# Kernel tuning notes

Measured on AMD Instinct MI355X. Metric: run time of the kernel, lower is better.

Reference implementation:

```python
import jax, jax.numpy as jnp
import numpy as np

D_MODEL = 1024
N_HEADS = 16
D_K = D_MODEL // N_HEADS


def setup_inputs() -> dict:
    key = jax.random.key(0)
    ks = jax.random.split(key, 7)
    B, S, D = 2, 2048, D_MODEL
    scale = 1.0 / np.sqrt(D)
    return {
        "query": jax.random.normal(ks[0], (B, S, D), dtype=jnp.float32),
        "key": jax.random.normal(ks[1], (B, S, D), dtype=jnp.float32),
        "value": jax.random.normal(ks[2], (B, S, D), dtype=jnp.float32),
        "w_q": jax.random.normal(ks[3], (D, D), dtype=jnp.float32) * scale,
        "w_k": jax.random.normal(ks[4], (D, D), dtype=jnp.float32) * scale,
        "w_v": jax.random.normal(ks[5], (D, D), dtype=jnp.float32) * scale,
        "w_o": jax.random.normal(ks[6], (D, D), dtype=jnp.float32) * scale,
    }


def reference(query, key, value, w_q, w_k, w_v, w_o):
    B, S, D = query.shape
    H, Dk = N_HEADS, D_K
    # nn.Linear (no bias): x @ W.T ; then split heads -> [B, H, S, Dk]
    def split_heads(x, W):
        return (x @ W.T).reshape(B, S, H, Dk).transpose(0, 2, 1, 3)
    Q = split_heads(query, w_q)
    K = split_heads(key, w_k)
    V = split_heads(value, w_v)
    scores = jnp.einsum("bhqd,bhkd->bhqk", Q, K) / np.sqrt(Dk).astype(jnp.float32)
    attn = jax.nn.softmax(scores, axis=-1)  # dropout is identity in eval
    attended = jnp.einsum("bhqk,bhkd->bhqd", attn, V)
    attended = attended.transpose(0, 2, 1, 3).reshape(B, S, D)
    output = attended @ w_o.T
    avg_attention = attn.mean(axis=1)  # mean over heads -> [B, S, S]
    return (output, avg_attention)
```

## Files before the change

### kernel.cpp

```cpp
#include <hip/hip_runtime.h>
#include <math.h>

#define SEQ 2048
#define DMODEL 1024
#define NH 16
#define DK 64
#define BATCH 2

using bf16x8 = __attribute__((ext_vector_type(8))) __bf16;
using bf16x4 = __attribute__((ext_vector_type(4))) __bf16;
using f32x4  = __attribute__((ext_vector_type(4))) float;

__device__ inline f32x4 mfma16(bf16x8 a, bf16x8 b, f32x4 c) {
    return __builtin_amdgcn_mfma_f32_16x16x32_bf16(a, b, c, 0, 0, 0);
}

__device__ inline void load_lds16(const void* g, void* l) {
    __builtin_amdgcn_global_load_lds(
        (const __attribute__((address_space(1))) void*)g,
        (__attribute__((address_space(3))) void*)l, 16, 0, 0);
}

#define EXP_SCALE 0.18033688011112042f

__global__ __launch_bounds__(256) void conv_bf16(
        const float* __restrict__ q, const float* __restrict__ k,
        const float* __restrict__ v, const float* __restrict__ wq,
        const float* __restrict__ wk, const float* __restrict__ wv,
        const float* __restrict__ wo,
        __bf16* __restrict__ oq, __bf16* __restrict__ ok, __bf16* __restrict__ ov,
        __bf16* __restrict__ owq, __bf16* __restrict__ owk,
        __bf16* __restrict__ owv, __bf16* __restrict__ owo) {
    int bid = blockIdx.x;
    const float* src;
    __bf16* dst;
    size_t off;
    if (bid < 3072) {
        int ti = bid >> 10;
        src = ti == 0 ? q : (ti == 1 ? k : v);
        dst = ti == 0 ? oq : (ti == 1 ? ok : ov);
        off = (size_t)(bid & 1023) * 4096;
    } else {
        int ti = (bid - 3072) >> 8;
        src = ti == 0 ? wq : (ti == 1 ? wk : (ti == 2 ? wv : wo));
        dst = ti == 0 ? owq : (ti == 1 ? owk : (ti == 2 ? owv : owo));
        off = (size_t)((bid - 3072) & 255) * 4096;
    }
    src += off; dst += off;
    const int t = threadIdx.x;
#pragma unroll
    for (int i = 0; i < 4; ++i) {
        float4 x = *(const float4*)(src + t * 4 + i * 1024);
        bf16x4 y;
        y[0] = (__bf16)x.x; y[1] = (__bf16)x.y;
        y[2] = (__bf16)x.z; y[3] = (__bf16)x.w;
        *(bf16x4*)(dst + t * 4 + i * 1024) = y;
    }
}

__device__ __forceinline__ void gemm_core(const __bf16* __restrict__ A,
                                          const __bf16* __restrict__ B,
                                          void* __restrict__ out, int mode,
                                          int m0, int n0, int N,
                                          __bf16* As, __bf16* Bs) {
    const int t    = threadIdx.x;
    const int w    = t >> 6;
    const int lane = t & 63;
    const int m    = lane & 15;
    const int kg   = lane >> 4;
    const int wr   = w >> 1, wc = w & 1;

    f32x4 acc[4][2] = {};

    for (int k0 = 0; k0 < 1024; k0 += 64) {
        __syncthreads();
#pragma unroll
        for (int i = 0; i < 4; ++i) {
            const int ablk = w * 4 + i;
            const int mt = ablk >> 1, kt = ablk & 1;
            const __bf16* ga = A + (size_t)(m0 + mt * 16 + m) * 1024 + k0 + kt * 32 + kg * 8;
            load_lds16(ga, &As[ablk * 512]);
        }
#pragma unroll
        for (int i = 0; i < 2; ++i) {
            const int bblk = w * 2 + i;
            const int nt = bblk >> 1, kt = bblk & 1;
            const __bf16* gb = B + (size_t)(n0 + nt * 16 + m) * 1024 + k0 + kt * 32 + kg * 8;
            load_lds16(gb, &Bs[bblk * 512]);
        }
        __syncthreads();
#pragma unroll
        for (int kt = 0; kt < 2; ++kt) {
            bf16x8 af[4], bg[2];
#pragma unroll
            for (int i = 0; i < 4; ++i)
                af[i] = *(const bf16x8*)&As[((wr * 4 + i) * 2 + kt) * 512 + lane * 8];
#pragma unroll
            for (int j = 0; j < 2; ++j)
                bg[j] = *(const bf16x8*)&Bs[((wc * 2 + j) * 2 + kt) * 512 + lane * 8];
#pragma unroll
            for (int i = 0; i < 4; ++i)
#pragma unroll
                for (int j = 0; j < 2; ++j)
                    acc[i][j] = mfma16(af[i], bg[j], acc[i][j]);
        }
    }

#pragma unroll
    for (int i = 0; i < 4; ++i) {
        const int rb = m0 + wr * 64 + i * 16 + kg * 4;
#pragma unroll
        for (int j = 0; j < 2; ++j) {
            const int gc = n0 + wc * 32 + j * 16 + m;
#pragma unroll
            for (int r = 0; r < 4; ++r) {
                const int gr = rb + r;
                const float vv = acc[i][j][r];
                if (mode == 0) {
                    ((float*)out)[(size_t)gr * N + gc] = vv;
                } else if (mode == 1) {
                    ((__bf16*)out)[(size_t)gr * N + gc] = (__bf16)vv;
                } else {
                    const int hh = gr >> 6, dd = gr & 63;
                    const int bb = gc >> 11, ss = gc & 2047;
                    ((__bf16*)out)[(((size_t)bb * NH + hh) * DK + dd) * SEQ + ss] = (__bf16)vv;
                }
            }
        }
    }
}

__device__ __forceinline__ int xcd_swz(int s, int cpx) {
    return (s & 7) * cpx + (s >> 3);
}

__global__ __launch_bounds__(256) void gemm_qkv(
        const __bf16* __restrict__ Xq, const __bf16* __restrict__ Wq, __bf16* Qr,
        const __bf16* __restrict__ Xk, const __bf16* __restrict__ Wk, __bf16* Kr,
        const __bf16* __restrict__ Xv, const __bf16* __restrict__ Wv, __bf16* Vt) {
    __shared__ __align__(16) __bf16 As[8192];
    __shared__ __align__(16) __bf16 Bs[4096];
    const int bid = blockIdx.x;
    if (bid < 512) {
        const int s = xcd_swz(bid, 64);
        gemm_core(Xq, Wq, Qr, 1, (s >> 4) * 128, (s & 15) * 64, 1024, As, Bs);
    } else if (bid < 1024) {
        const int s = xcd_swz(bid - 512, 64);
        gemm_core(Xk, Wk, Kr, 1, (s >> 4) * 128, (s & 15) * 64, 1024, As, Bs);
    } else {
        const int s = xcd_swz(bid - 1024, 64);
        gemm_core(Wv, Xv, Vt, 2, (s >> 6) * 128, (s & 63) * 64, 4096, As, Bs);
    }
}

__global__ __launch_bounds__(512) void attn_flash(const __bf16* __restrict__ Qr,
                                                  const __bf16* __restrict__ Kr,
                                                  const __bf16* __restrict__ Vt,
                                                  __bf16* __restrict__ att,
                                                  float* __restrict__ invs) {
    __shared__ __align__(16) unsigned char smem[49664];
    __bf16* KbA  = (__bf16*)smem;
    __bf16* VbA  = KbA + 8192;
    __bf16* PbA  = VbA + 8192;
    float*  sinv = (float*)(smem + 49152);

    const int t    = threadIdx.x;
    const int w    = t >> 6;
    const int lane = t & 63;
    const int m    = lane & 15;
    const int kg   = lane >> 4;

    const int L  = xcd_swz(blockIdx.x, 64);
    const int b  = L >> 8;
    const int h  = (L >> 4) & 15;
    const int qw = (L & 15) * 128 + w * 16;

    const __bf16* Kh = Kr + (size_t)b * SEQ * 1024 + h * 64;
    const __bf16* Vh = Vt + ((size_t)b * NH + h) * DK * SEQ;
    __bf16* Pw = PbA + w * 1024;

    const size_t rowQ = (size_t)(b * SEQ + qw + m) * 1024 + h * 64 + kg * 8;
    const bf16x8 qa = *(const bf16x8*)(Qr + rowQ);
    const bf16x8 qb = *(const bf16x8*)(Qr + rowQ + 32);

    const int srow = t >> 3;
    const int su   = t & 7;
    const int sus  = (su ^ (srow & 7)) * 8;
    auto stage = [&](int buf, int kt) {
        load_lds16(Kh + (size_t)(kt + srow) * 1024 + sus, KbA + buf * 4096 + w * 512);
        load_lds16(Vh + (size_t)srow * SEQ + kt + sus,    VbA + buf * 4096 + w * 512);
    };

    f32x4 pv[4] = {};
    float rsum = 0.f;

    stage(0, 0);
    __syncthreads();

    int cur = 0;
    for (int kt = 0; kt < SEQ; kt += 64) {
        if (kt + 64 < SEQ) stage(cur ^ 1, kt + 64);
        const __bf16* Kc = KbA + cur * 4096;
        const __bf16* Vc = VbA + cur * 4096;
#pragma unroll
        for (int nt = 0; nt < 4; ++nt) {
            const int row = nt * 16 + m;
            bf16x8 k0 = *(const bf16x8*)&Kc[row * 64 + ((kg ^ (m & 7)) * 8)];
            bf16x8 k1 = *(const bf16x8*)&Kc[row * 64 + (((kg + 4) ^ (m & 7)) * 8)];
            f32x4 c = {};
            c = mfma16(k0, qa, c);
            c = mfma16(k1, qb, c);
            bf16x4 pk;
#pragma unroll
            for (int r = 0; r < 4; ++r) {
                float p = exp2f(c[r] * EXP_SCALE);
                rsum += p;
                pk[r] = (__bf16)p;
            }
            const int off8  = nt * 4 + kg;
            const int off8s = (((off8 >> 1) ^ (m & 7)) << 1) | (off8 & 1);
            *(bf16x4*)&Pw[m * 64 + off8s * 4] = pk;
        }
#pragma unroll
        for (int ks = 0; ks < 2; ++ks) {
            const int u = (ks * 4 + kg) ^ (m & 7);
            bf16x8 pa = *(const bf16x8*)&Pw[m * 64 + u * 8];
#pragma unroll
            for (int nt = 0; nt < 4; ++nt) {
                bf16x8 vb = *(const bf16x8*)&Vc[(nt * 16 + m) * 64 + u * 8];
                pv[nt] = mfma16(pa, vb, pv[nt]);
            }
        }
        __syncthreads();
        cur ^= 1;
    }

    rsum += __shfl_xor(rsum, 16);
    rsum += __shfl_xor(rsum, 32);
    const float inv = 1.0f / rsum;
    if (lane < 16) {
        sinv[w * 16 + m] = inv;
        invs[((size_t)b * NH + h) * SEQ + qw + m] = inv;
    }
    __syncthreads();
    float iv[4];
#pragma unroll
    for (int r = 0; r < 4; ++r) iv[r] = sinv[w * 16 + kg * 4 + r];

    float* scf = (float*)smem + w * 1088;
#pragma unroll
    for (int nt = 0; nt < 4; ++nt)
#pragma unroll
        for (int r = 0; r < 4; ++r)
            scf[(kg * 4 + r) * 68 + nt * 16 + m] = pv[nt][r] * iv[r];
    __syncthreads();
    {
        const int q = lane >> 2, c0 = (lane & 3) * 16;
        const float* srcf = &scf[q * 68 + c0];
        bf16x8 o0, o1;
#pragma unroll
        for (int j = 0; j < 8; ++j) {
            o0[j] = (__bf16)srcf[j];
            o1[j] = (__bf16)srcf[j + 8];
        }
        __bf16* dst = att + (size_t)(b * SEQ + qw + q) * DMODEL + h * DK + c0;
        *(bf16x8*)(dst)     = o0;
        *(bf16x8*)(dst + 8) = o1;
    }
}

__device__ __forceinline__ void avg_core(const __bf16* __restrict__ Qr,
                                         const __bf16* __restrict__ Kr,
                                         const float* __restrict__ invs,
                                         float* __restrict__ avg,
                                         int L, __bf16* Kb) {
    const int t    = threadIdx.x;
    const int w    = t >> 6;
    const int lane = t & 63;
    const int m    = lane & 15;
    const int kg   = lane >> 4;
    const int b    = L >> 9;
    const int s0   = ((L >> 5) & 15) * 128;
    const int qw   = (L & 31) * 64 + w * 16;

    const __bf16* Kbase = Kr + (size_t)(b * SEQ + s0) * 1024;

    auto stageK = [&](int buf, int h) {
#pragma unroll
        for (int s = 0; s < 4; ++s) {
            const int i   = w * 4 + s;
            const int row = i * 8 + (lane >> 3);
            const int u   = lane & 7;
            load_lds16(Kbase + (size_t)row * 1024 + h * 64 + ((u ^ (row & 7)) * 8),
                       Kb + buf * 8192 + i * 512);
        }
    };

    f32x4 acc[8] = {};

    stageK(0, 0);
    const size_t qoff = (size_t)(b * SEQ + qw + m) * 1024 + kg * 8;
    bf16x8 a0 = *(const bf16x8*)(Qr + qoff);
    bf16x8 a1 = *(const bf16x8*)(Qr + qoff + 32);
    f32x4 ivr = *(const f32x4*)&invs[(size_t)b * NH * SEQ + qw + kg * 4];
    __syncthreads();

    int cur = 0;
    for (int h = 0; h < NH; ++h) {
        if (h + 1 < NH) stageK(cur ^ 1, h + 1);
        bf16x8 na0, na1;
        f32x4 nivr;
        if (h + 1 < NH) {
            na0  = *(const bf16x8*)(Qr + qoff + (h + 1) * 64);
            na1  = *(const bf16x8*)(Qr + qoff + (h + 1) * 64 + 32);
            nivr = *(const f32x4*)&invs[((size_t)b * NH + h + 1) * SEQ + qw + kg * 4];
        }
        const __bf16* Kc = Kb + cur * 8192;
#pragma unroll
        for (int nt = 0; nt < 8; ++nt) {
            const int row = nt * 16 + m;
            bf16x8 k0 = *(const bf16x8*)&Kc[row * 64 + ((kg ^ (m & 7)) * 8)];
            bf16x8 k1 = *(const bf16x8*)&Kc[row * 64 + (((kg + 4) ^ (m & 7)) * 8)];
            f32x4 c = {};
            c = mfma16(a0, k0, c);
            c = mfma16(a1, k1, c);
#pragma unroll
            for (int r = 0; r < 4; ++r)
                acc[nt][r] += ivr[r] * exp2f(c[r] * EXP_SCALE);
        }
        __syncthreads();
        cur ^= 1;
        a0 = na0; a1 = na1; ivr = nivr;
    }

    const float sc = 1.0f / NH;
#pragma unroll
    for (int nt = 0; nt < 8; ++nt)
#pragma unroll
        for (int r = 0; r < 4; ++r)
            avg[(size_t)(b * SEQ + qw + kg * 4 + r) * SEQ + s0 + nt * 16 + m] =
                acc[nt][r] * sc;
}

__global__ __launch_bounds__(256) void gemm_wo_avg(
        const __bf16* __restrict__ At, const __bf16* __restrict__ Wo,
        float* __restrict__ out,
        const __bf16* __restrict__ Qr, const __bf16* __restrict__ Kr,
        const float* __restrict__ invs, float* __restrict__ avg) {
    __shared__ __align__(16) __bf16 sm[16384];
    const int bid = blockIdx.x;
    if (bid < 512) {
        const int s = xcd_swz(bid, 64);
        gemm_core(At, Wo, out, 0, (s >> 4) * 128, (s & 15) * 64, 1024,
                  sm, sm + 8192);
    } else {
        avg_core(Qr, Kr, invs, avg, xcd_swz(bid - 512, 128), sm);
    }
}

extern "C" void kernel_launch(void* const* d_in, const int* in_sizes, int n_in,
                              void* d_out, int out_size, void* d_ws, size_t ws_size,
                              hipStream_t stream) {
    const float* query = (const float*)d_in[0];
    const float* key   = (const float*)d_in[1];
    const float* value = (const float*)d_in[2];
    const float* w_q   = (const float*)d_in[3];
    const float* w_k   = (const float*)d_in[4];
    const float* w_v   = (const float*)d_in[5];
    const float* w_o   = (const float*)d_in[6];

    float* out = (float*)d_out;
    float* avg = out + (size_t)BATCH * SEQ * DMODEL;

    __bf16* Xq = (__bf16*)d_ws;
    __bf16* Xk = Xq + 4194304;
    __bf16* Xv = Xk + 4194304;
    __bf16* Wq = Xv + 4194304;
    __bf16* Wk = Wq + 1048576;
    __bf16* Wv = Wk + 1048576;
    __bf16* Wo = Wv + 1048576;
    __bf16* Qr = Wo + 1048576;
    __bf16* Kr = Qr + 4194304;
    __bf16* Vt = Kr + 4194304;
    float*  Invs = (float*)(Vt + 4194304);
    __bf16* At = Xq;

    conv_bf16<<<4096, 256, 0, stream>>>(query, key, value, w_q, w_k, w_v, w_o,
                                        Xq, Xk, Xv, Wq, Wk, Wv, Wo);

    gemm_qkv<<<1536, 256, 0, stream>>>(Xq, Wq, Qr, Xk, Wk, Kr, Xv, Wv, Vt);

    attn_flash<<<512, 512, 0, stream>>>(Qr, Kr, Vt, At, Invs);

    gemm_wo_avg<<<1536, 256, 0, stream>>>(At, Wo, out, Qr, Kr, Invs, avg);
}
```

Measured before the change: 310.8 us.

## Use 128-wide key tiles with register-staged prefetch and native exp2 in attention

```diff
diff --git a/kernel.cpp b/kernel.cpp
--- a/kernel.cpp
+++ b/kernel.cpp
@@ -21,7 +21,9 @@
         (__attribute__((address_space(3))) void*)l, 16, 0, 0);
 }
 
+#define BARRIER() __builtin_amdgcn_s_barrier()
 #define EXP_SCALE 0.18033688011112042f
+#define EXP2(x) __builtin_amdgcn_exp2f(x)
 
 __global__ __launch_bounds__(256) void conv_bf16(
         const float* __restrict__ q, const float* __restrict__ k,
@@ -153,16 +155,16 @@
     }
 }
 
-__global__ __launch_bounds__(512) void attn_flash(const __bf16* __restrict__ Qr,
-                                                  const __bf16* __restrict__ Kr,
-                                                  const __bf16* __restrict__ Vt,
-                                                  __bf16* __restrict__ att,
-                                                  float* __restrict__ invs) {
-    __shared__ __align__(16) unsigned char smem[49664];
-    __bf16* KbA  = (__bf16*)smem;
-    __bf16* VbA  = KbA + 8192;
-    __bf16* PbA  = VbA + 8192;
-    float*  sinv = (float*)(smem + 49152);
+__global__ __launch_bounds__(512, 4) void attn_flash(const __bf16* __restrict__ Qr,
+                                                     const __bf16* __restrict__ Kr,
+                                                     const __bf16* __restrict__ Vt,
+                                                     __bf16* __restrict__ att,
+                                                     float* __restrict__ invs) {
+    __shared__ __align__(16) unsigned char smem[66048];
+    __bf16* Ks   = (__bf16*)smem;
+    __bf16* Vs   = (__bf16*)(smem + 16384);
+    __bf16* Pb   = (__bf16*)(smem + 32768);
+    float*  sinv = (float*)(smem + 65536);
 
     const int t    = threadIdx.x;
     const int w    = t >> 6;
@@ -177,62 +179,75 @@
 
     const __bf16* Kh = Kr + (size_t)b * SEQ * 1024 + h * 64;
     const __bf16* Vh = Vt + ((size_t)b * NH + h) * DK * SEQ;
-    __bf16* Pw = PbA + w * 1024;
+    __bf16* Pw = Pb + w * 2048;
 
     const size_t rowQ = (size_t)(b * SEQ + qw + m) * 1024 + h * 64 + kg * 8;
     const bf16x8 qa = *(const bf16x8*)(Qr + rowQ);
     const bf16x8 qb = *(const bf16x8*)(Qr + rowQ + 32);
 
-    const int srow = t >> 3;
-    const int su   = t & 7;
-    const int sus  = (su ^ (srow & 7)) * 8;
-    auto stage = [&](int buf, int kt) {
-        load_lds16(Kh + (size_t)(kt + srow) * 1024 + sus, KbA + buf * 4096 + w * 512);
-        load_lds16(Vh + (size_t)srow * SEQ + kt + sus,    VbA + buf * 4096 + w * 512);
+    const int rk0 = t >> 3,          ck0 = t & 7;
+    const int rk1 = (t + 512) >> 3,  ck1 = (t + 512) & 7;
+    const int rv0 = t >> 4,          cv0 = t & 15;
+    const int rv1 = (t + 512) >> 4,  cv1 = (t + 512) & 15;
+    bf16x8 kst0, kst1, vst0, vst1;
+
+    auto issue = [&](int kt) {
+        kst0 = *(const bf16x8*)(Kh + (size_t)(kt + rk0) * 1024 + ck0 * 8);
+        kst1 = *(const bf16x8*)(Kh + (size_t)(kt + rk1) * 1024 + ck1 * 8);
+        vst0 = *(const bf16x8*)(Vh + (size_t)rv0 * SEQ + kt + cv0 * 8);
+        vst1 = *(const bf16x8*)(Vh + (size_t)rv1 * SEQ + kt + cv1 * 8);
+    };
+    auto commit = [&]() {
+        *(bf16x8*)&Ks[rk0 * 64 + ((ck0 ^ (rk0 & 7)) * 8)] = kst0;
+        *(bf16x8*)&Ks[rk1 * 64 + ((ck1 ^ (rk1 & 7)) * 8)] = kst1;
+        *(bf16x8*)&Vs[rv0 * 128 + ((cv0 ^ (rv0 & 7)) * 8)] = vst0;
+        *(bf16x8*)&Vs[rv1 * 128 + ((cv1 ^ (rv1 & 7)) * 8)] = vst1;
     };
 
     f32x4 pv[4] = {};
     float rsum = 0.f;
 
-    stage(0, 0);
+    issue(0);
+    commit();
     __syncthreads();
 
-    int cur = 0;
-    for (int kt = 0; kt < SEQ; kt += 64) {
-        if (kt + 64 < SEQ) stage(cur ^ 1, kt + 64);
-        const __bf16* Kc = KbA + cur * 4096;
-        const __bf16* Vc = VbA + cur * 4096;
-#pragma unroll
-        for (int nt = 0; nt < 4; ++nt) {
+    for (int kt = 0; kt < SEQ; kt += 128) {
+        if (kt + 128 < SEQ) issue(kt + 128);
+#pragma unroll
+        for (int nt = 0; nt < 8; ++nt) {
             const int row = nt * 16 + m;
-            bf16x8 k0 = *(const bf16x8*)&Kc[row * 64 + ((kg ^ (m & 7)) * 8)];
-            bf16x8 k1 = *(const bf16x8*)&Kc[row * 64 + (((kg + 4) ^ (m & 7)) * 8)];
+            bf16x8 k0 = *(const bf16x8*)&Ks[row * 64 + ((kg ^ (m & 7)) * 8)];
+            bf16x8 k1 = *(const bf16x8*)&Ks[row * 64 + (((kg + 4) ^ (m & 7)) * 8)];
             f32x4 c = {};
             c = mfma16(k0, qa, c);
             c = mfma16(k1, qb, c);
             bf16x4 pk;
 #pragma unroll
             for (int r = 0; r < 4; ++r) {
-                float p = exp2f(c[r] * EXP_SCALE);
+                float p = EXP2(c[r] * EXP_SCALE);
                 rsum += p;
                 pk[r] = (__bf16)p;
             }
-            const int off8  = nt * 4 + kg;
-            const int off8s = (((off8 >> 1) ^ (m & 7)) << 1) | (off8 & 1);
-            *(bf16x4*)&Pw[m * 64 + off8s * 4] = pk;
-        }
-#pragma unroll
-        for (int ks = 0; ks < 2; ++ks) {
+            const int up = (nt * 2 + (kg >> 1)) ^ (m & 7);
+            *(bf16x4*)&Pw[m * 128 + (((up << 1) | (kg & 1)) * 4)] = pk;
+        }
+#pragma unroll
+        for (int ks = 0; ks < 4; ++ks) {
             const int u = (ks * 4 + kg) ^ (m & 7);
-            bf16x8 pa = *(const bf16x8*)&Pw[m * 64 + u * 8];
+            bf16x8 pa = *(const bf16x8*)&Pw[m * 128 + u * 8];
 #pragma unroll
             for (int nt = 0; nt < 4; ++nt) {
-                bf16x8 vb = *(const bf16x8*)&Vc[(nt * 16 + m) * 64 + u * 8];
+                const int rv = nt * 16 + m;
+                bf16x8 vb = *(const bf16x8*)&Vs[rv * 128 + u * 8];
                 pv[nt] = mfma16(pa, vb, pv[nt]);
             }
         }
         __syncthreads();
-        cur ^= 1;
+        if (kt + 128 < SEQ) {
+            commit();
+            asm volatile("s_waitcnt lgkmcnt(0)" ::: "memory");
+            BARRIER();
+        }
     }
 
     rsum += __shfl_xor(rsum, 16);
@@ -326,7 +341,7 @@
             c = mfma16(a1, k1, c);
 #pragma unroll
             for (int r = 0; r < 4; ++r)
-                acc[nt][r] += ivr[r] * exp2f(c[r] * EXP_SCALE);
+                acc[nt][r] += ivr[r] * EXP2(c[r] * EXP_SCALE);
         }
         __syncthreads();
         cur ^= 1;
```

Measured after the change: 292.2 us. 6.0% less time.
